# Kernel tuning notes

Measured on AMD Instinct MI355X. Metric: run time of the kernel, lower is better.

## Reference

```python
import jax, jax.numpy as jnp
import numpy as np

B, L, D = 1024, 30, 300   # batch, title length, total_dim
H, HD = 20, 20            # num_heads, head_dim
VOCAB = 30000


def _xavier_uniform(key, shape):
    # torch nn.init.xavier_uniform_ on a 3D tensor [H, din, dout*]:
    # fan_in = size(1) * prod(size(2:)), fan_out = size(0) * prod(size(2:))
    receptive = int(np.prod(shape[2:])) if len(shape) > 2 else 1
    fan_in = shape[1] * receptive
    fan_out = shape[0] * receptive
    bound = float(np.sqrt(6.0 / (fan_in + fan_out)))
    return jax.random.uniform(key, shape, jnp.float32, -bound, bound)


def setup_inputs() -> dict:
    key = jax.random.key(0)
    k_y, k_seq, k_q, k_v = jax.random.split(key, 4)
    y = jax.random.normal(k_y, (B, L, D), jnp.float32)
    seq = jax.random.randint(k_seq, (B, L), 0, VOCAB, jnp.int64)
    Q = _xavier_uniform(k_q, (H, D, D))
    V = _xavier_uniform(k_v, (H, D, HD))
    return {"y": y, "sequences_input_title": seq, "Q": Q, "V": V}


def reference(y, sequences_input_title, Q, V):
    # mask over key positions: [B, 1, 1, L]
    mask = (sequences_input_title > 0).astype(y.dtype)[:, None, None, :]
    # per-head query projection: [B, H, L, D]
    a1 = jnp.einsum('bld,hde->bhle', y, Q)
    # raw scores: [B, H, L, L]
    a2 = jnp.einsum('bhle,bme->bhlm', a1, y)
    a3 = jnp.exp(a2)  # NOTE: no max-subtraction, faithful to source
    # denominator uses masked scores, numerator does NOT (faithful bug-for-bug)
    a5 = jnp.sum(a3 * mask, axis=-1, keepdims=True) + 1e-6
    alpha = a3 / a5
    # weighted values then per-head output projection
    h0 = jnp.einsum('bhlm,bmd->bhld', alpha, y)
    h1 = jnp.einsum('bhld,hdf->bhlf', h0, V)     # [B, H, L, HD]
    # concat heads along last dim (head-major blocks, matching torch.cat)
    return h1.transpose(0, 2, 1, 3).reshape(y.shape[0], y.shape[1], -1)
```

## Files before the change

kernel.cpp:

```cpp
#include <hip/hip_runtime.h>
#include <math.h>

#define Bb 1024
#define Ll 30
#define Dd 300
#define Hh 20
#define HDd 20

typedef __attribute__((ext_vector_type(8))) short short8;
typedef __attribute__((ext_vector_type(4))) float f32x4;

#define SW(row, col) ((row)*320 + ((((col) >> 3) ^ ((row) & 7)) << 3) + ((col) & 7))

#define QELEMS (Hh*19*10*64*8)
#define VELEMS (Hh*2*10*64*8)
#define WS_NEEDED ((size_t)(2*QELEMS + 2*VELEMS) * 2)

__device__ __forceinline__ void bf16split(float x, unsigned short& h, unsigned short& l) {
    unsigned u = __float_as_uint(x);
    unsigned hr = (u + 0x7FFFu + ((u >> 16) & 1u)) >> 16;
    float hf = __uint_as_float(hr << 16);
    float r = x - hf;
    unsigned v = __float_as_uint(r);
    unsigned lr = (v + 0x7FFFu + ((v >> 16) & 1u)) >> 16;
    h = (unsigned short)hr; l = (unsigned short)lr;
}
__device__ __forceinline__ unsigned short rne16(float x) {
    unsigned u = __float_as_uint(x);
    return (unsigned short)((u + 0x7FFFu + ((u >> 16) & 1u)) >> 16);
}

__global__ void pack_q(const float* __restrict__ Q,
                       unsigned short* __restrict__ qh, unsigned short* __restrict__ ql) {
    int g = blockIdx.x * blockDim.x + threadIdx.x;
    if (g >= Hh*19*10*64) return;
    int l = g & 63;
    int t = g >> 6;
    int ks = t % 10; t /= 10;
    int nt = t % 19; int h = t / 19;
    int e = 16*nt + (l & 15);
    int kbase = 32*ks + 8*(l >> 4);
    unsigned hp[4], lp[4];
    #pragma unroll
    for (int p = 0; p < 4; ++p) {
        int k0 = kbase + 2*p, k1 = k0 + 1;
        float x0 = (k0 < Dd && e < Dd) ? Q[h*Dd*Dd + k0*Dd + e] : 0.f;
        float x1 = (k1 < Dd && e < Dd) ? Q[h*Dd*Dd + k1*Dd + e] : 0.f;
        unsigned short h0,l0,h1,l1;
        bf16split(x0,h0,l0); bf16split(x1,h1,l1);
        hp[p] = (unsigned)h0 | ((unsigned)h1 << 16);
        lp[p] = (unsigned)l0 | ((unsigned)l1 << 16);
    }
    ((uint4*)qh)[g] = make_uint4(hp[0],hp[1],hp[2],hp[3]);
    ((uint4*)ql)[g] = make_uint4(lp[0],lp[1],lp[2],lp[3]);
}

__global__ void pack_v(const float* __restrict__ V,
                       unsigned short* __restrict__ vh, unsigned short* __restrict__ vl) {
    int g = blockIdx.x * blockDim.x + threadIdx.x;
    if (g >= Hh*2*10*64) return;
    int l = g & 63;
    int t = g >> 6;
    int ks = t % 10; t /= 10;
    int nt = t % 2; int h = t / 2;
    int f = 16*nt + (l & 15);
    int kbase = 32*ks + 8*(l >> 4);
    unsigned hp[4], lp[4];
    #pragma unroll
    for (int p = 0; p < 4; ++p) {
        int k0 = kbase + 2*p, k1 = k0 + 1;
        float x0 = (k0 < Dd && f < HDd) ? V[h*Dd*HDd + k0*HDd + f] : 0.f;
        float x1 = (k1 < Dd && f < HDd) ? V[h*Dd*HDd + k1*HDd + f] : 0.f;
        unsigned short h0,l0,h1,l1;
        bf16split(x0,h0,l0); bf16split(x1,h1,l1);
        hp[p] = (unsigned)h0 | ((unsigned)h1 << 16);
        lp[p] = (unsigned)l0 | ((unsigned)l1 << 16);
    }
    ((uint4*)vh)[g] = make_uint4(hp[0],hp[1],hp[2],hp[3]);
    ((uint4*)vl)[g] = make_uint4(lp[0],lp[1],lp[2],lp[3]);
}

__global__ __launch_bounds__(512, 2)
void mha_v4(const float* __restrict__ y, const int* __restrict__ seq,
            const unsigned short* __restrict__ qh, const unsigned short* __restrict__ ql,
            const unsigned short* __restrict__ vh, const unsigned short* __restrict__ vl,
            float* __restrict__ out)
{
    __shared__ __align__(16) unsigned short y_h[32*320], y_l[32*320];
    __shared__ __align__(16) unsigned short a1h[32*320], a1l[32*320];

    const int bid = blockIdx.x;
    const int h = bid >> 10, b = bid & 1023;
    const int tid = threadIdx.x;
    const int lane = tid & 63, wid = tid >> 6;
    const int lrow = lane & 15, lk = lane >> 4;
    const int l7 = lrow & 7;

    const float* yb = y + (size_t)b * (Ll * Dd);
    for (int idx = tid; idx < 32*320; idx += 512) {
        int row = idx / 320, col = idx - row*320;
        float v = (row < Ll && col < Dd) ? yb[row*Dd + col] : 0.f;
        unsigned short hv, lv; bf16split(v, hv, lv);
        int sidx = SW(row, col);
        y_h[sidx] = hv; y_l[sidx] = lv;
    }
    if (tid < 128) {
        int r = tid & 31, c = 38 + ((tid >> 5) & 1);
        unsigned short* p = (tid >> 6) ? a1l : a1h;
        int sc = c ^ (r & 7);
        *((uint4*)&p[r*320 + sc*8]) = make_uint4(0,0,0,0);
    }
    __syncthreads();

    for (int nt = wid; nt < 19; nt += 8) {
        f32x4 acc[2][2];
        #pragma unroll
        for (int i = 0; i < 2; ++i) { acc[i][0] = (f32x4){0,0,0,0}; acc[i][1] = (f32x4){0,0,0,0}; }
        const unsigned short* qhp = qh + (size_t)((h*19 + nt)*10)*512 + lane*8;
        const unsigned short* qlp = ql + (size_t)((h*19 + nt)*10)*512 + lane*8;
        #pragma unroll 2
        for (int ks = 0; ks < 10; ++ks) {
            short8 bh = *(const short8*)(qhp + ks*512);
            short8 bl = *(const short8*)(qlp + ks*512);
            const int ch = ((4*ks + lk) ^ l7) << 3;
            #pragma unroll
            for (int Mt = 0; Mt < 2; ++Mt) {
                int ia = (16*Mt + lrow)*320 + ch;
                short8 ah = *(const short8*)&y_h[ia];
                short8 al = *(const short8*)&y_l[ia];
                acc[Mt][ks&1] = __builtin_amdgcn_mfma_f32_16x16x32_bf16(ah, bh, acc[Mt][ks&1], 0,0,0);
                acc[Mt][ks&1] = __builtin_amdgcn_mfma_f32_16x16x32_bf16(al, bh, acc[Mt][ks&1], 0,0,0);
                acc[Mt][ks&1] = __builtin_amdgcn_mfma_f32_16x16x32_bf16(ah, bl, acc[Mt][ks&1], 0,0,0);
            }
        }
        #pragma unroll
        for (int Mt = 0; Mt < 2; ++Mt) {
            f32x4 a = acc[Mt][0] + acc[Mt][1];
            #pragma unroll
            for (int r = 0; r < 4; ++r) {
                int row = 16*Mt + 4*lk + r;
                int col = 16*nt + lrow;
                unsigned short hv, lv; bf16split(a[r], hv, lv);
                int sidx = SW(row, col);
                a1h[sidx] = hv;
                a1l[sidx] = lv;
            }
        }
    }
    __syncthreads();

    f32x4 Pacc = (f32x4){0,0,0,0};
    float alf[2][4];

    if (wid < 2) {
        const int Mt = wid;
        f32x4 acc[2][2];
        #pragma unroll
        for (int i = 0; i < 2; ++i) { acc[i][0] = (f32x4){0,0,0,0}; acc[i][1] = (f32x4){0,0,0,0}; }
        #pragma unroll 2
        for (int ntp = 0; ntp < 10; ++ntp) {
            const int ch = ((4*ntp + lk) ^ l7) << 3;
            int ia = (16*Mt + lrow)*320 + ch;
            short8 ah = *(const short8*)&a1h[ia];
            short8 al = *(const short8*)&a1l[ia];
            #pragma unroll
            for (int Nt = 0; Nt < 2; ++Nt) {
                int ib = (16*Nt + lrow)*320 + ch;
                short8 bh = *(const short8*)&y_h[ib];
                short8 bl = *(const short8*)&y_l[ib];
                acc[Nt][ntp&1] = __builtin_amdgcn_mfma_f32_16x16x32_bf16(ah, bh, acc[Nt][ntp&1], 0,0,0);
                acc[Nt][ntp&1] = __builtin_amdgcn_mfma_f32_16x16x32_bf16(al, bh, acc[Nt][ntp&1], 0,0,0);
                acc[Nt][ntp&1] = __builtin_amdgcn_mfma_f32_16x16x32_bf16(ah, bl, acc[Nt][ntp&1], 0,0,0);
            }
        }
        f32x4 S0 = acc[0][0] + acc[0][1];
        f32x4 S1 = acc[1][0] + acc[1][1];
        const float mk0 = (seq[b*Ll + lrow] > 0) ? 1.f : 0.f;
        const float mk1 = (lrow < 14) ? ((seq[b*Ll + 16 + lrow] > 0) ? 1.f : 0.f) : 0.f;
        #pragma unroll
        for (int r = 0; r < 4; ++r) {
            float s0 = S0[r], s1 = S1[r];
            float v = fmaxf(s0, (lrow < 14) ? s1 : -3.4e38f);
            #pragma unroll
            for (int off = 8; off >= 1; off >>= 1)
                v = fmaxf(v, __shfl_xor(v, off, 64));
            float e0 = __expf(s0 - v);
            float e1 = __expf(s1 - v);
            float sum = e0 * mk0 + e1 * mk1;
            #pragma unroll
            for (int off = 8; off >= 1; off >>= 1)
                sum += __shfl_xor(sum, off, 64);
            float denom = sum + 1e-6f * __expf(-v);
            alf[0][r] = e0 / denom;
            alf[1][r] = (lrow < 14) ? e1 / denom : 0.f;
        }
    } else if (wid < 6) {
        const int w = wid - 2, Mtp = w >> 1, Ntp = w & 1;
        f32x4 acc[2];
        acc[0] = (f32x4){0,0,0,0}; acc[1] = (f32x4){0,0,0,0};
        const unsigned short* vhp = vh + (size_t)((h*2 + Ntp)*10)*512 + lane*8;
        const unsigned short* vlp = vl + (size_t)((h*2 + Ntp)*10)*512 + lane*8;
        #pragma unroll 2
        for (int ks = 0; ks < 10; ++ks) {
            short8 bh = *(const short8*)(vhp + ks*512);
            short8 bl = *(const short8*)(vlp + ks*512);
            int ia = (16*Mtp + lrow)*320 + (((4*ks + lk) ^ l7) << 3);
            short8 ah = *(const short8*)&y_h[ia];
            short8 al = *(const short8*)&y_l[ia];
            acc[ks&1] = __builtin_amdgcn_mfma_f32_16x16x32_bf16(ah, bh, acc[ks&1], 0,0,0);
            acc[ks&1] = __builtin_amdgcn_mfma_f32_16x16x32_bf16(al, bh, acc[ks&1], 0,0,0);
            acc[ks&1] = __builtin_amdgcn_mfma_f32_16x16x32_bf16(ah, bl, acc[ks&1], 0,0,0);
        }
        Pacc = acc[0] + acc[1];
    }
    __syncthreads();

    if (wid < 2) {
        const int Mt = wid;
        #pragma unroll
        for (int Nt = 0; Nt < 2; ++Nt)
            #pragma unroll
            for (int r = 0; r < 4; ++r)
                a1l[SW(16*Mt + 4*lk + r, 16*Nt + lrow)] = rne16(alf[Nt][r]);
    } else if (wid < 6) {
        const int w = wid - 2, Mtp = w >> 1, Ntp = w & 1;
        #pragma unroll
        for (int r = 0; r < 4; ++r)
            a1h[SW(16*Ntp + lrow, 16*Mtp + 4*lk + r)] = rne16(Pacc[r]);
    }
    __syncthreads();

    if (wid < 4) {
        const int Mt = wid >> 1, Nt = wid & 1;
        short8 af = *(const short8*)&a1l[(16*Mt + lrow)*320 + ((lk ^ l7) << 3)];
        short8 pf = *(const short8*)&a1h[(16*Nt + lrow)*320 + ((lk ^ l7) << 3)];
        f32x4 O = __builtin_amdgcn_mfma_f32_16x16x32_bf16(af, pf, (f32x4){0,0,0,0}, 0,0,0);
        #pragma unroll
        for (int r = 0; r < 4; ++r) {
            int q = 16*Mt + 4*lk + r;
            int f = 16*Nt + lrow;
            if (q < Ll && f < HDd)
                out[(size_t)b*(Ll*Hh*HDd) + q*(Hh*HDd) + h*HDd + f] = O[r];
        }
    }
}

__global__ __launch_bounds__(256, 3)
void mha_fused_fp32(const float* __restrict__ y,
                    const int* __restrict__ seq,
                    const float* __restrict__ Q,
                    const float* __restrict__ V,
                    float* __restrict__ out)
{
    __shared__ float ys[32][320];
    __shared__ float alphaS[32][33];
    __shared__ float Plds[32][20];
    __shared__ float maskSf[32];

    const int bid = blockIdx.x;
    const int h = bid >> 10;
    const int b = bid & 1023;
    const int tid = threadIdx.x;
    const int tj = tid & 31;
    const int ti = tid >> 5;
    const int r0 = ti * 4;

    const float* yb = y + b * (Ll * Dd);
    for (int i = tid; i < 32 * 320; i += 256) {
        int row = i / 320;
        int col = i - row * 320;
        float v = 0.f;
        if (row < Ll && col < Dd) v = yb[row * Dd + col];
        ys[row][col] = v;
    }
    if (tid < 32) {
        float m = 0.f;
        if (tid < Ll) m = (seq[b * Ll + tid] > 0) ? 1.f : 0.f;
        maskSf[tid] = m;
    }
    __syncthreads();

    float a1reg[4][10];
    #pragma unroll
    for (int r = 0; r < 4; ++r)
        #pragma unroll
        for (int k = 0; k < 10; ++k) a1reg[r][k] = 0.f;

    const float* Qh = Q + h * (Dd * Dd) + tj;
    for (int d0 = 0; d0 < Dd; d0 += 4) {
        float ysv[4][4];
        #pragma unroll
        for (int r = 0; r < 4; ++r) {
            float4 t = *reinterpret_cast<const float4*>(&ys[r0 + r][d0]);
            ysv[r][0] = t.x; ysv[r][1] = t.y; ysv[r][2] = t.z; ysv[r][3] = t.w;
        }
        #pragma unroll
        for (int dd = 0; dd < 4; ++dd) {
            const float* qp = Qh + (d0 + dd) * Dd;
            float qv[10];
            #pragma unroll
            for (int k = 0; k < 9; ++k) qv[k] = qp[32 * k];
            qv[9] = (tj < 12) ? qp[288] : 0.f;
            #pragma unroll
            for (int r = 0; r < 4; ++r) {
                float yd = ysv[r][dd];
                #pragma unroll
                for (int k = 0; k < 10; ++k)
                    a1reg[r][k] = fmaf(yd, qv[k], a1reg[r][k]);
            }
        }
    }

    float Sreg[4] = {0.f, 0.f, 0.f, 0.f};
    for (int m = 0; m < Ll; ++m) {
        float yv[10];
        #pragma unroll
        for (int k = 0; k < 10; ++k) yv[k] = ys[m][tj + 32 * k];
        float part[4];
        #pragma unroll
        for (int r = 0; r < 4; ++r) {
            float s = 0.f;
            #pragma unroll
            for (int k = 0; k < 10; ++k) s = fmaf(a1reg[r][k], yv[k], s);
            part[r] = s;
        }
        #pragma unroll
        for (int off = 16; off >= 1; off >>= 1)
            #pragma unroll
            for (int r = 0; r < 4; ++r)
                part[r] += __shfl_xor(part[r], off, 64);
        #pragma unroll
        for (int r = 0; r < 4; ++r)
            if (tj == m) Sreg[r] = part[r];
    }

    const float maskv = maskSf[tj];
    float Areg[4];
    #pragma unroll
    for (int r = 0; r < 4; ++r) {
        float v = (tj < Ll) ? Sreg[r] : -3.4e38f;
        #pragma unroll
        for (int off = 16; off >= 1; off >>= 1)
            v = fmaxf(v, __shfl_xor(v, off, 64));
        float e = __expf(Sreg[r] - v);
        float s = (tj < Ll) ? e * maskv : 0.f;
        #pragma unroll
        for (int off = 16; off >= 1; off >>= 1)
            s += __shfl_xor(s, off, 64);
        float denom = s + 1e-6f * __expf(-v);
        Areg[r] = e / denom;
    }
    #pragma unroll
    for (int r = 0; r < 4; ++r)
        if (r0 + r < Ll && tj < Ll) alphaS[r0 + r][tj] = Areg[r];

    float Pacc[4] = {0.f, 0.f, 0.f, 0.f};
    if (tj < HDd) {
        const float* Vh = V + h * (Dd * HDd) + tj;
        for (int d0 = 0; d0 < Dd; d0 += 4) {
            float ysv[4][4];
            #pragma unroll
            for (int r = 0; r < 4; ++r) {
                float4 t = *reinterpret_cast<const float4*>(&ys[r0 + r][d0]);
                ysv[r][0] = t.x; ysv[r][1] = t.y; ysv[r][2] = t.z; ysv[r][3] = t.w;
            }
            float vv[4];
            #pragma unroll
            for (int dd = 0; dd < 4; ++dd) vv[dd] = Vh[(d0 + dd) * HDd];
            #pragma unroll
            for (int r = 0; r < 4; ++r)
                #pragma unroll
                for (int dd = 0; dd < 4; ++dd)
                    Pacc[r] = fmaf(ysv[r][dd], vv[dd], Pacc[r]);
        }
    }
    #pragma unroll
    for (int r = 0; r < 4; ++r)
        if (tj < HDd && r0 + r < Ll) Plds[r0 + r][tj] = Pacc[r];
    __syncthreads();

    float* outb = out + b * (Ll * Hh * HDd) + h * HDd;
    for (int t = tid; t < Ll * HDd; t += 256) {
        int l = t / HDd;
        int f = t - l * HDd;
        float acc = 0.f;
        #pragma unroll
        for (int m = 0; m < Ll; ++m)
            acc = fmaf(alphaS[l][m], Plds[m][f], acc);
        outb[l * (Hh * HDd) + f] = acc;
    }
}

extern "C" void kernel_launch(void* const* d_in, const int* in_sizes, int n_in,
                              void* d_out, int out_size, void* d_ws, size_t ws_size,
                              hipStream_t stream) {
    (void)in_sizes; (void)n_in; (void)out_size;
    const float* y   = (const float*)d_in[0];
    const int*   seq = (const int*)d_in[1];
    const float* Q   = (const float*)d_in[2];
    const float* V   = (const float*)d_in[3];
    float* out = (float*)d_out;

    if (ws_size < WS_NEEDED) {
        hipLaunchKernelGGL(mha_fused_fp32, dim3(Bb * Hh), dim3(256), 0, stream, y, seq, Q, V, out);
        return;
    }

    unsigned short* qh = (unsigned short*)d_ws;
    unsigned short* ql = qh + QELEMS;
    unsigned short* vh = ql + QELEMS;
    unsigned short* vl = vh + VELEMS;

    pack_q<<<dim3((Hh*19*10*64 + 255)/256), dim3(256), 0, stream>>>(Q, qh, ql);
    pack_v<<<dim3((Hh*2*10*64 + 255)/256), dim3(256), 0, stream>>>(V, vh, vl);
    mha_v4<<<dim3(Bb * Hh), dim3(512), 0, stream>>>(y, seq, qh, ql, vh, vl, out);
}
```

Before: 782.2 us.

## Vectorize y staging, split Q-projection tiles per wave, use hardware bf16 convert

```diff
diff --git a/kernel.cpp b/kernel.cpp
--- a/kernel.cpp
+++ b/kernel.cpp
@@ -1,4 +1,5 @@
 #include <hip/hip_runtime.h>
+#include <hip/hip_bf16.h>
 #include <math.h>
 
 #define Bb 1024
@@ -9,6 +10,7 @@
 
 typedef __attribute__((ext_vector_type(8))) short short8;
 typedef __attribute__((ext_vector_type(4))) float f32x4;
+typedef __attribute__((ext_vector_type(4))) unsigned short u16x4;
 
 #define SW(row, col) ((row)*320 + ((((col) >> 3) ^ ((row) & 7)) << 3) + ((col) & 7))
 
@@ -16,6 +18,14 @@
 #define VELEMS (Hh*2*10*64*8)
 #define WS_NEEDED ((size_t)(2*QELEMS + 2*VELEMS) * 2)
 
+__device__ __forceinline__ unsigned short cvt_hi(float x) {
+    return __builtin_bit_cast(unsigned short, __float2bfloat16(x));
+}
+__device__ __forceinline__ void splitc(float x, unsigned short& h, unsigned short& l) {
+    h = cvt_hi(x);
+    float hf = __uint_as_float((unsigned)h << 16);
+    l = cvt_hi(x - hf);
+}
 __device__ __forceinline__ void bf16split(float x, unsigned short& h, unsigned short& l) {
     unsigned u = __float_as_uint(x);
     unsigned hr = (u + 0x7FFFu + ((u >> 16) & 1u)) >> 16;
@@ -24,10 +34,6 @@
     unsigned v = __float_as_uint(r);
     unsigned lr = (v + 0x7FFFu + ((v >> 16) & 1u)) >> 16;
     h = (unsigned short)hr; l = (unsigned short)lr;
-}
-__device__ __forceinline__ unsigned short rne16(float x) {
-    unsigned u = __float_as_uint(x);
-    return (unsigned short)((u + 0x7FFFu + ((u >> 16) & 1u)) >> 16);
 }
 
 __global__ void pack_q(const float* __restrict__ Q,
@@ -81,7 +87,7 @@
 }
 
 __global__ __launch_bounds__(512, 2)
-void mha_v4(const float* __restrict__ y, const int* __restrict__ seq,
+void mha_v5(const float* __restrict__ y, const int* __restrict__ seq,
             const unsigned short* __restrict__ qh, const unsigned short* __restrict__ ql,
             const unsigned short* __restrict__ vh, const unsigned short* __restrict__ vl,
             float* __restrict__ out)
@@ -97,12 +103,22 @@
     const int l7 = lrow & 7;
 
     const float* yb = y + (size_t)b * (Ll * Dd);
-    for (int idx = tid; idx < 32*320; idx += 512) {
-        int row = idx / 320, col = idx - row*320;
-        float v = (row < Ll && col < Dd) ? yb[row*Dd + col] : 0.f;
-        unsigned short hv, lv; bf16split(v, hv, lv);
-        int sidx = SW(row, col);
-        y_h[sidx] = hv; y_l[sidx] = lv;
+    const float4 z4 = make_float4(0.f, 0.f, 0.f, 0.f);
+    for (int idx4 = tid; idx4 < 32*80; idx4 += 512) {
+        int row = idx4 / 80;
+        int c4  = (idx4 - row*80) << 2;
+        float4 v = (row < Ll && c4 < Dd) ? *reinterpret_cast<const float4*>(yb + row*Dd + c4) : z4;
+        unsigned short h0, l0, h1, l1, h2, l2, h3, l3;
+        splitc(v.x, h0, l0);
+        splitc(v.y, h1, l1);
+        splitc(v.z, h2, l2);
+        splitc(v.w, h3, l3);
+        u16x4 hv, lv;
+        hv[0] = h0; hv[1] = h1; hv[2] = h2; hv[3] = h3;
+        lv[0] = l0; lv[1] = l1; lv[2] = l2; lv[3] = l3;
+        int sidx = SW(row, c4);
+        *reinterpret_cast<u16x4*>(&y_h[sidx]) = hv;
+        *reinterpret_cast<u16x4*>(&y_l[sidx]) = lv;
     }
     if (tid < 128) {
         int r = tid & 31, c = 38 + ((tid >> 5) & 1);
@@ -112,39 +128,38 @@
     }
     __syncthreads();
 
-    for (int nt = wid; nt < 19; nt += 8) {
-        f32x4 acc[2][2];
-        #pragma unroll
-        for (int i = 0; i < 2; ++i) { acc[i][0] = (f32x4){0,0,0,0}; acc[i][1] = (f32x4){0,0,0,0}; }
+    for (int ht = wid; ht < 38; ht += 8) {
+        const int nt = ht >> 1, Mt = ht & 1;
+        f32x4 acc0 = (f32x4){0,0,0,0}, acc1 = (f32x4){0,0,0,0};
         const unsigned short* qhp = qh + (size_t)((h*19 + nt)*10)*512 + lane*8;
         const unsigned short* qlp = ql + (size_t)((h*19 + nt)*10)*512 + lane*8;
-        #pragma unroll 2
+        const int arow = (16*Mt + lrow)*320;
+        #pragma unroll
         for (int ks = 0; ks < 10; ++ks) {
             short8 bh = *(const short8*)(qhp + ks*512);
             short8 bl = *(const short8*)(qlp + ks*512);
-            const int ch = ((4*ks + lk) ^ l7) << 3;
-            #pragma unroll
-            for (int Mt = 0; Mt < 2; ++Mt) {
-                int ia = (16*Mt + lrow)*320 + ch;
-                short8 ah = *(const short8*)&y_h[ia];
-                short8 al = *(const short8*)&y_l[ia];
-                acc[Mt][ks&1] = __builtin_amdgcn_mfma_f32_16x16x32_bf16(ah, bh, acc[Mt][ks&1], 0,0,0);
-                acc[Mt][ks&1] = __builtin_amdgcn_mfma_f32_16x16x32_bf16(al, bh, acc[Mt][ks&1], 0,0,0);
-                acc[Mt][ks&1] = __builtin_amdgcn_mfma_f32_16x16x32_bf16(ah, bl, acc[Mt][ks&1], 0,0,0);
+            const int ia = arow + (((4*ks + lk) ^ l7) << 3);
+            short8 ah = *(const short8*)&y_h[ia];
+            short8 al = *(const short8*)&y_l[ia];
+            if (ks & 1) {
+                acc1 = __builtin_amdgcn_mfma_f32_16x16x32_bf16(ah, bh, acc1, 0,0,0);
+                acc1 = __builtin_amdgcn_mfma_f32_16x16x32_bf16(al, bh, acc1, 0,0,0);
+                acc1 = __builtin_amdgcn_mfma_f32_16x16x32_bf16(ah, bl, acc1, 0,0,0);
+            } else {
+                acc0 = __builtin_amdgcn_mfma_f32_16x16x32_bf16(ah, bh, acc0, 0,0,0);
+                acc0 = __builtin_amdgcn_mfma_f32_16x16x32_bf16(al, bh, acc0, 0,0,0);
+                acc0 = __builtin_amdgcn_mfma_f32_16x16x32_bf16(ah, bl, acc0, 0,0,0);
             }
         }
-        #pragma unroll
-        for (int Mt = 0; Mt < 2; ++Mt) {
-            f32x4 a = acc[Mt][0] + acc[Mt][1];
-            #pragma unroll
-            for (int r = 0; r < 4; ++r) {
-                int row = 16*Mt + 4*lk + r;
-                int col = 16*nt + lrow;
-                unsigned short hv, lv; bf16split(a[r], hv, lv);
-                int sidx = SW(row, col);
-                a1h[sidx] = hv;
-                a1l[sidx] = lv;
-            }
+        f32x4 a = acc0 + acc1;
+        const int col = 16*nt + lrow;
+        #pragma unroll
+        for (int r = 0; r < 4; ++r) {
+            int row = 16*Mt + 4*lk + r;
+            unsigned short hv, lv; splitc(a[r], hv, lv);
+            int sidx = SW(row, col);
+            a1h[sidx] = hv;
+            a1l[sidx] = lv;
         }
     }
     __syncthreads();
@@ -157,12 +172,12 @@
         f32x4 acc[2][2];
         #pragma unroll
         for (int i = 0; i < 2; ++i) { acc[i][0] = (f32x4){0,0,0,0}; acc[i][1] = (f32x4){0,0,0,0}; }
-        #pragma unroll 2
+        const int arow = (16*Mt + lrow)*320;
+        #pragma unroll
         for (int ntp = 0; ntp < 10; ++ntp) {
             const int ch = ((4*ntp + lk) ^ l7) << 3;
-            int ia = (16*Mt + lrow)*320 + ch;
-            short8 ah = *(const short8*)&a1h[ia];
-            short8 al = *(const short8*)&a1l[ia];
+            short8 ah = *(const short8*)&a1h[arow + ch];
+            short8 al = *(const short8*)&a1l[arow + ch];
             #pragma unroll
             for (int Nt = 0; Nt < 2; ++Nt) {
                 int ib = (16*Nt + lrow)*320 + ch;
@@ -196,22 +211,28 @@
         }
     } else if (wid < 6) {
         const int w = wid - 2, Mtp = w >> 1, Ntp = w & 1;
-        f32x4 acc[2];
-        acc[0] = (f32x4){0,0,0,0}; acc[1] = (f32x4){0,0,0,0};
+        f32x4 acc0 = (f32x4){0,0,0,0}, acc1 = (f32x4){0,0,0,0};
         const unsigned short* vhp = vh + (size_t)((h*2 + Ntp)*10)*512 + lane*8;
         const unsigned short* vlp = vl + (size_t)((h*2 + Ntp)*10)*512 + lane*8;
-        #pragma unroll 2
+        const int arow = (16*Mtp + lrow)*320;
+        #pragma unroll
         for (int ks = 0; ks < 10; ++ks) {
             short8 bh = *(const short8*)(vhp + ks*512);
             short8 bl = *(const short8*)(vlp + ks*512);
-            int ia = (16*Mtp + lrow)*320 + (((4*ks + lk) ^ l7) << 3);
+            int ia = arow + (((4*ks + lk) ^ l7) << 3);
             short8 ah = *(const short8*)&y_h[ia];
             short8 al = *(const short8*)&y_l[ia];
-            acc[ks&1] = __builtin_amdgcn_mfma_f32_16x16x32_bf16(ah, bh, acc[ks&1], 0,0,0);
-            acc[ks&1] = __builtin_amdgcn_mfma_f32_16x16x32_bf16(al, bh, acc[ks&1], 0,0,0);
-            acc[ks&1] = __builtin_amdgcn_mfma_f32_16x16x32_bf16(ah, bl, acc[ks&1], 0,0,0);
-        }
-        Pacc = acc[0] + acc[1];
+            if (ks & 1) {
+                acc1 = __builtin_amdgcn_mfma_f32_16x16x32_bf16(ah, bh, acc1, 0,0,0);
+                acc1 = __builtin_amdgcn_mfma_f32_16x16x32_bf16(al, bh, acc1, 0,0,0);
+                acc1 = __builtin_amdgcn_mfma_f32_16x16x32_bf16(ah, bl, acc1, 0,0,0);
+            } else {
+                acc0 = __builtin_amdgcn_mfma_f32_16x16x32_bf16(ah, bh, acc0, 0,0,0);
+                acc0 = __builtin_amdgcn_mfma_f32_16x16x32_bf16(al, bh, acc0, 0,0,0);
+                acc0 = __builtin_amdgcn_mfma_f32_16x16x32_bf16(ah, bl, acc0, 0,0,0);
+            }
+        }
+        Pacc = acc0 + acc1;
     }
     __syncthreads();
 
@@ -221,12 +242,12 @@
         for (int Nt = 0; Nt < 2; ++Nt)
             #pragma unroll
             for (int r = 0; r < 4; ++r)
-                a1l[SW(16*Mt + 4*lk + r, 16*Nt + lrow)] = rne16(alf[Nt][r]);
+                a1l[SW(16*Mt + 4*lk + r, 16*Nt + lrow)] = cvt_hi(alf[Nt][r]);
     } else if (wid < 6) {
         const int w = wid - 2, Mtp = w >> 1, Ntp = w & 1;
         #pragma unroll
         for (int r = 0; r < 4; ++r)
-            a1h[SW(16*Ntp + lrow, 16*Mtp + 4*lk + r)] = rne16(Pacc[r]);
+            a1h[SW(16*Ntp + lrow, 16*Mtp + 4*lk + r)] = cvt_hi(Pacc[r]);
     }
     __syncthreads();
 
@@ -413,5 +434,5 @@
 
     pack_q<<<dim3((Hh*19*10*64 + 255)/256), dim3(256), 0, stream>>>(Q, qh, ql);
     pack_v<<<dim3((Hh*2*10*64 + 255)/256), dim3(256), 0, stream>>>(V, vh, vl);
-    mha_v4<<<dim3(Bb * Hh), dim3(512), 0, stream>>>(y, seq, qh, ql, vh, vl, out);
-}
+    mha_v5<<<dim3(Bb * Hh), dim3(512), 0, stream>>>(y, seq, qh, ql, vh, vl, out);
+}
```

Measured after the change: 708.3 us (median of 5 runs). 1.1x faster.
